# Performance work log

Measured on AMD Instinct MI355X. Metric: run time of the kernel, lower is better.

## Reference

```python
import jax, jax.numpy as jnp
import numpy as np

E, H, I = 8, 2048, 768  # num_experts, hidden_size, moe_intermediate_size
B, S = 4, 1024


def setup_inputs() -> dict:
    key = jax.random.key(0)
    k1, k2, k3, k4, k5 = jax.random.split(key, 5)
    hidden_states = jax.random.normal(k1, (B, S, H), dtype=jnp.float32)
    routing_weights = jax.random.uniform(k2, (B * S, E), dtype=jnp.float32)
    router_indices = jax.random.randint(k3, (B * S, 2), 0, E)
    gate_up_proj = jax.random.normal(k4, (E, H, 2 * I), dtype=jnp.float32) * 0.02
    down_proj = jax.random.normal(k5, (E, I, H), dtype=jnp.float32) * 0.02
    return {
        "hidden_states": hidden_states,
        "routing_weights": routing_weights,
        "router_indices": router_indices,
        "gate_up_proj": gate_up_proj,
        "down_proj": down_proj,
    }


def reference(hidden_states, routing_weights, router_indices, gate_up_proj, down_proj):
    b, s, h = hidden_states.shape
    x = hidden_states.reshape(-1, h)  # [T, H], T = B*S
    # dense all-experts: every token through every expert
    gate_up = jnp.einsum("th,ehd->etd", x, gate_up_proj)  # [E, T, 2I]
    gate, up = jnp.split(gate_up, 2, axis=-1)
    inter = up * jax.nn.silu(gate)  # [E, T, I]
    out = jnp.einsum("eti,eih->eth", inter, down_proj)  # [E, T, H]
    rw = routing_weights.T.reshape(out.shape[0], b, s)  # [E, B, S]
    out = out.reshape(out.shape[0], b, s, h) * rw[..., None]
    return out.sum(axis=0)  # [B, S, H]
```

## Files before the change

### kernel.cpp

```cpp
#include <hip/hip_runtime.h>
#include <cstdint>
#include <cstddef>

#define NE 8
#define NH 2048
#define NI 768
#define NT 4096
#define NK2 6144

typedef __bf16 bf16x8 __attribute__((ext_vector_type(8)));
typedef float f32x4 __attribute__((ext_vector_type(4)));
typedef unsigned short u16x8 __attribute__((ext_vector_type(8)));

__device__ __forceinline__ unsigned short f2bf(float f) {
  unsigned int u = __builtin_bit_cast(unsigned int, f);
  u += 0x7fffu + ((u >> 16) & 1u);
  return (unsigned short)(u >> 16);
}

__device__ __forceinline__ void gload_lds16(const void* g, void* s) {
  __builtin_amdgcn_global_load_lds(
      (const __attribute__((address_space(1))) unsigned int*)g,
      (__attribute__((address_space(3))) unsigned int*)s, 16, 0, 0);
}

__global__ __launch_bounds__(256) void k_cvt(const float* __restrict__ in,
                                             unsigned short* __restrict__ out,
                                             long n) {
  long i = ((long)blockIdx.x * blockDim.x + threadIdx.x) * 8;
  if (i >= n) return;
  float4 f0 = *reinterpret_cast<const float4*>(in + i);
  float4 f1 = *reinterpret_cast<const float4*>(in + i + 4);
  u16x8 o;
  o[0] = f2bf(f0.x); o[1] = f2bf(f0.y); o[2] = f2bf(f0.z); o[3] = f2bf(f0.w);
  o[4] = f2bf(f1.x); o[5] = f2bf(f1.y); o[6] = f2bf(f1.z); o[7] = f2bf(f1.w);
  *reinterpret_cast<u16x8*>(out + i) = o;
}

__global__ __launch_bounds__(256) void k_transpose_cvt(
    const float* __restrict__ in, unsigned short* __restrict__ out,
    int R, int C, long inBS, long outBS, int outCS, int mode) {
  __shared__ float tile[32][33];
  const int b = blockIdx.z;
  const int r0 = blockIdx.y * 32, c0 = blockIdx.x * 32;
  const int tx = threadIdx.x, ty = threadIdx.y;
  const float* ib = in + (long)b * inBS;
#pragma unroll
  for (int d = 0; d < 4; d++)
    tile[ty + d * 8][tx] = ib[(long)(r0 + ty + d * 8) * C + c0 + tx];
  __syncthreads();
#pragma unroll
  for (int d = 0; d < 4; d++) {
    int c = c0 + ty + d * 8;
    int r = r0 + tx;
    int orow;
    if (mode == 1) {
      int z = (c >= NI) ? 1 : 0;
      int cc = c - z * NI;
      orow = ((cc >> 4) << 5) + (z << 4) + (cc & 15);
    } else {
      orow = c;
    }
    out[(long)b * outBS + (long)orow * outCS + r] = f2bf(tile[tx][ty + d * 8]);
  }
}


__global__ __launch_bounds__(512, 1) void k_gemm1(
    const unsigned short* __restrict__ Xb,
    const unsigned short* __restrict__ W1t,
    const float* __restrict__ rw,
    unsigned short* __restrict__ inter) {
  __shared__ unsigned short ldsA[2][16384];
  __shared__ unsigned short ldsB[2][16384];

  const int e = blockIdx.z;
  const int t0 = blockIdx.y * 256;
  const int bn = blockIdx.x;
  const int tid = threadIdx.x;
  const int lane = tid & 63, wave = tid >> 6;
  const int wr = wave >> 2, wc = wave & 3;
  const int fr = lane & 15, fq = lane >> 4;
  const int nkt = NH / 64;

  const unsigned short* Bg = W1t + (size_t)e * (2 * NI) * NH;
  const int rih = tid >> 3, ck = tid & 7;
  const unsigned short* sA = Xb + (size_t)(t0 + rih) * NH + ((ck ^ (rih & 7)) << 3);
  const unsigned short* sB = Bg + (size_t)(bn * 256 + rih) * NH + ((ck ^ (rih & 7)) << 3);
  const int dst = tid * 8;

#define STG1(C) do { \
    const int cc_ = (C); const size_t ko_ = (size_t)cc_ * 64; \
    unsigned short* da_ = &ldsA[cc_ & 1][dst]; \
    unsigned short* db_ = &ldsB[cc_ & 1][dst]; \
    _Pragma("unroll") \
    for (int q = 0; q < 4; ++q) { \
      gload_lds16(sA + ko_ + (size_t)q * (64 * NH), da_ + q * 4096); \
      gload_lds16(sB + ko_ + (size_t)q * (64 * NH), db_ + q * 4096); \
    } \
  } while (0)

  f32x4 acc[8][4];
#pragma unroll
  for (int i = 0; i < 8; ++i)
#pragma unroll
    for (int j = 0; j < 4; ++j) acc[i][j] = (f32x4){0.f, 0.f, 0.f, 0.f};

  const int swz = fr & 7;
  int aoff[8], boff[4];
#pragma unroll
  for (int i = 0; i < 8; ++i)
    aoff[i] = ((i >> 2) * 128 + wr * 64 + (i & 3) * 16 + fr) * 64 + ((fq ^ swz) << 3);
#pragma unroll
  for (int j = 0; j < 4; ++j)
    boff[j] = ((j >> 1) * 128 + wc * 32 + (j & 1) * 16 + fr) * 64 + ((fq ^ swz) << 3);
  const int dk = ((((4 + fq) ^ swz) - (fq ^ swz)) << 3);

  STG1(0);
  asm volatile("s_waitcnt vmcnt(0)" ::: "memory");
  asm volatile("s_barrier" ::: "memory");

  for (int kt = 0; kt < nkt; ++kt) {
    const int cur = kt & 1;
    const unsigned short* lA = ldsA[cur];
    const unsigned short* lB = ldsB[cur];

    bf16x8 af[8][2], bf[4][2];
#pragma unroll
    for (int m = 0; m < 8; ++m) {
      af[m][0] = *reinterpret_cast<const bf16x8*>(lA + aoff[m]);
      af[m][1] = *reinterpret_cast<const bf16x8*>(lA + aoff[m] + dk);
    }
#pragma unroll
    for (int j = 0; j < 4; ++j) {
      bf[j][0] = *reinterpret_cast<const bf16x8*>(lB + boff[j]);
      bf[j][1] = *reinterpret_cast<const bf16x8*>(lB + boff[j] + dk);
    }

    if (kt + 1 < nkt) STG1(kt + 1);

#pragma unroll
    for (int kk = 0; kk < 2; ++kk)
#pragma unroll
      for (int m = 0; m < 8; ++m)
#pragma unroll
        for (int j = 0; j < 4; ++j)
          acc[m][j] = __builtin_amdgcn_mfma_f32_16x16x32_bf16(af[m][kk], bf[j][kk], acc[m][j], 0, 0, 0);

    asm volatile("s_waitcnt vmcnt(0)" ::: "memory");
    asm volatile("s_barrier" ::: "memory");
  }
#undef STG1

#pragma unroll
  for (int i = 0; i < 8; ++i) {
    const int trow = t0 + (i >> 2) * 128 + wr * 64 + (i & 3) * 16 + fq * 4;
#pragma unroll
    for (int r = 0; r < 4; ++r) {
      const int t = trow + r;
      const float rwv = rw[(size_t)t * NE + e];
#pragma unroll
      for (int p = 0; p < 2; ++p) {
        float g = acc[i][2 * p][r];
        float u = acc[i][2 * p + 1][r];
        float s = g / (1.f + __expf(-g));
        const int col = bn * 128 + (p * 4 + wc) * 16 + fr;
        inter[(size_t)t * NK2 + e * NI + col] = f2bf(rwv * u * s);
      }
    }
  }
}

__global__ __launch_bounds__(512, 1) void k_gemm2(
    const unsigned short* __restrict__ inter,
    const unsigned short* __restrict__ W2t,
    float* __restrict__ out) {
  __shared__ unsigned short ldsA[2][16384];
  __shared__ unsigned short ldsB[2][8192];

  const int t0 = blockIdx.y * 256;
  const int h0 = blockIdx.x * 128;
  const int tid = threadIdx.x;
  const int lane = tid & 63, wave = tid >> 6;
  const int wr = wave >> 1, wc = wave & 1;
  const int fr = lane & 15, fq = lane >> 4;
  const int nkt = NK2 / 64;

  const int rih = tid >> 3, ck = tid & 7;
  const unsigned short* sA = inter + (size_t)(t0 + rih) * NK2 + ((ck ^ (rih & 7)) << 3);
  const unsigned short* sB = W2t + (size_t)(h0 + rih) * NK2 + ((ck ^ (rih & 7)) << 3);
  const int dst = tid * 8;

#define STG2(C) do { \
    const int cc_ = (C); \
    unsigned short* da_ = &ldsA[cc_ & 1][dst]; \
    unsigned short* db_ = &ldsB[cc_ & 1][dst]; \
    const size_t ko_ = (size_t)cc_ * 64; \
    _Pragma("unroll") \
    for (int q = 0; q < 4; ++q) \
      gload_lds16(sA + ko_ + (size_t)q * (64 * NK2), da_ + q * 4096); \
    _Pragma("unroll") \
    for (int q = 0; q < 2; ++q) \
      gload_lds16(sB + ko_ + (size_t)q * (64 * NK2), db_ + q * 4096); \
  } while (0)

  f32x4 acc[4][4];
#pragma unroll
  for (int i = 0; i < 4; ++i)
#pragma unroll
    for (int j = 0; j < 4; ++j) acc[i][j] = (f32x4){0.f, 0.f, 0.f, 0.f};

  const int swz = fr & 7;
  int aoff[4], boff[4];
#pragma unroll
  for (int i = 0; i < 4; ++i)
    aoff[i] = (wr * 64 + i * 16 + fr) * 64 + ((fq ^ swz) << 3);
#pragma unroll
  for (int j = 0; j < 4; ++j)
    boff[j] = (wc * 64 + j * 16 + fr) * 64 + ((fq ^ swz) << 3);
  const int dk = ((((4 + fq) ^ swz) - (fq ^ swz)) << 3);

  STG2(0);
  asm volatile("s_waitcnt vmcnt(0)" ::: "memory");
  asm volatile("s_barrier" ::: "memory");

  for (int kt = 0; kt < nkt; ++kt) {
    const int cur = kt & 1;
    const unsigned short* lA = ldsA[cur];
    const unsigned short* lB = ldsB[cur];

    bf16x8 af[4][2], bf[4][2];
#pragma unroll
    for (int i = 0; i < 4; ++i) {
      af[i][0] = *reinterpret_cast<const bf16x8*>(lA + aoff[i]);
      af[i][1] = *reinterpret_cast<const bf16x8*>(lA + aoff[i] + dk);
    }
#pragma unroll
    for (int j = 0; j < 4; ++j) {
      bf[j][0] = *reinterpret_cast<const bf16x8*>(lB + boff[j]);
      bf[j][1] = *reinterpret_cast<const bf16x8*>(lB + boff[j] + dk);
    }

    if (kt + 1 < nkt) STG2(kt + 1);

#pragma unroll
    for (int kk = 0; kk < 2; ++kk)
#pragma unroll
      for (int i = 0; i < 4; ++i)
#pragma unroll
        for (int j = 0; j < 4; ++j)
          acc[i][j] = __builtin_amdgcn_mfma_f32_16x16x32_bf16(af[i][kk], bf[j][kk], acc[i][j], 0, 0, 0);

    asm volatile("s_waitcnt vmcnt(0)" ::: "memory");
    asm volatile("s_barrier" ::: "memory");
  }
#undef STG2

  const int rowBase = t0 + wr * 64 + fq * 4;
#pragma unroll
  for (int i = 0; i < 4; ++i)
#pragma unroll
    for (int j = 0; j < 4; ++j)
#pragma unroll
      for (int r = 0; r < 4; ++r)
        out[(size_t)(rowBase + i * 16 + r) * NH + h0 + wc * 64 + j * 16 + fr] =
            acc[i][j][r];
}

extern "C" void kernel_launch(void* const* d_in, const int* in_sizes, int n_in,
                              void* d_out, int out_size, void* d_ws, size_t ws_size,
                              hipStream_t stream) {
  const float* x = (const float*)d_in[0];
  const float* rw = (const float*)d_in[1];
  const float* w1 = (const float*)d_in[3];
  const float* w2 = (const float*)d_in[4];
  float* out = (float*)d_out;

  char* ws = (char*)d_ws;
  unsigned short* Xb = (unsigned short*)ws;
  unsigned short* W1t = (unsigned short*)(ws + 16777216);
  unsigned short* W2t = (unsigned short*)(ws + 16777216 + 50331648);
  unsigned short* inter = (unsigned short*)(ws + 16777216 + 50331648 + 25165824);

  k_cvt<<<dim3((NT * NH) / (256 * 8)), dim3(256), 0, stream>>>(x, Xb, (long)NT * NH);
  k_transpose_cvt<<<dim3((2 * NI) / 32, NH / 32, NE), dim3(32, 8), 0, stream>>>(
      w1, W1t, NH, 2 * NI, (long)NH * 2 * NI, (long)2 * NI * NH, NH, 1);
  k_transpose_cvt<<<dim3(NH / 32, NI / 32, NE), dim3(32, 8), 0, stream>>>(
      w2, W2t, NI, NH, (long)NI * NH, (long)NI, NK2, 0);
  k_gemm1<<<dim3((2 * NI) / 256, NT / 256, NE), dim3(512), 0, stream>>>(Xb, W1t, rw, inter);
  k_gemm2<<<dim3(NH / 128, NT / 256), dim3(512), 0, stream>>>(inter, W2t, out);
}
```

Baseline: 362.1 us.

## Deepen GEMM pipelines to 4-stage K=32 ring with register double-buffered fragments

Both GEMM kernels switch from a 2-stage, K=64 LDS double buffer with a full vmcnt(0) drain every iteration to a 4-slot LDS ring of K=32 tiles, prefetching three stages ahead. Fragment reads for the next step are issued before the MFMAs of the current step, and the wait uses partial vmcnt counts so global loads overlap compute. The LDS layout is changed to pack two rows per 64-element line with a new XOR swizzle. The cost is twice as many barriers per K, more registers for the two fragment sets, and a riskier wait and slot accounting scheme.

```diff
diff --git a/kernel.cpp b/kernel.cpp
--- a/kernel.cpp
+++ b/kernel.cpp
@@ -71,8 +71,7 @@
     const unsigned short* __restrict__ W1t,
     const float* __restrict__ rw,
     unsigned short* __restrict__ inter) {
-  __shared__ unsigned short ldsA[2][16384];
-  __shared__ unsigned short ldsB[2][16384];
+  __shared__ unsigned short lds[4][16384];
 
   const int e = blockIdx.z;
   const int t0 = blockIdx.y * 256;
@@ -81,23 +80,29 @@
   const int lane = tid & 63, wave = tid >> 6;
   const int wr = wave >> 2, wc = wave & 3;
   const int fr = lane & 15, fq = lane >> 4;
-  const int nkt = NH / 64;
+  const int nkt = NH / 32;
 
   const unsigned short* Bg = W1t + (size_t)e * (2 * NI) * NH;
-  const int rih = tid >> 3, ck = tid & 7;
-  const unsigned short* sA = Xb + (size_t)(t0 + rih) * NH + ((ck ^ (rih & 7)) << 3);
-  const unsigned short* sB = Bg + (size_t)(bn * 256 + rih) * NH + ((ck ^ (rih & 7)) << 3);
-  const int dst = tid * 8;
-
-#define STG1(C) do { \
-    const int cc_ = (C); const size_t ko_ = (size_t)cc_ * 64; \
-    unsigned short* da_ = &ldsA[cc_ & 1][dst]; \
-    unsigned short* db_ = &ldsB[cc_ & 1][dst]; \
-    _Pragma("unroll") \
-    for (int q = 0; q < 4; ++q) { \
-      gload_lds16(sA + ko_ + (size_t)q * (64 * NH), da_ + q * 4096); \
-      gload_lds16(sB + ko_ + (size_t)q * (64 * NH), db_ + q * 4096); \
-    } \
+
+  int r0c, k0c, r1c, k1c;
+  {
+    int c = tid, pr = c >> 3, pc = c & 7, pcl = pc ^ (pr & 7);
+    r0c = (pr << 1) | (pcl >> 2); k0c = pcl & 3;
+    c = tid + 512; pr = c >> 3; pc = c & 7; pcl = pc ^ (pr & 7);
+    r1c = (pr << 1) | (pcl >> 2); k1c = pcl & 3;
+  }
+  const unsigned short* sA0 = Xb + (size_t)(t0 + r0c) * NH + k0c * 8;
+  const unsigned short* sA1 = Xb + (size_t)(t0 + r1c) * NH + k1c * 8;
+  const unsigned short* sB0 = Bg + (size_t)(bn * 256 + r0c) * NH + k0c * 8;
+  const unsigned short* sB1 = Bg + (size_t)(bn * 256 + r1c) * NH + k1c * 8;
+  const int dst0 = tid * 8, dst1 = tid * 8 + 4096;
+
+#define STG1(T) do { \
+    unsigned short* L_ = lds[(T) & 3]; const size_t ko_ = (size_t)(T) * 32; \
+    gload_lds16(sA0 + ko_, L_ + dst0); \
+    gload_lds16(sA1 + ko_, L_ + dst1); \
+    gload_lds16(sB0 + ko_, L_ + 8192 + dst0); \
+    gload_lds16(sB1 + ko_, L_ + 8192 + dst1); \
   } while (0)
 
   f32x4 acc[8][4];
@@ -106,50 +111,57 @@
 #pragma unroll
     for (int j = 0; j < 4; ++j) acc[i][j] = (f32x4){0.f, 0.f, 0.f, 0.f};
 
-  const int swz = fr & 7;
   int aoff[8], boff[4];
 #pragma unroll
-  for (int i = 0; i < 8; ++i)
-    aoff[i] = ((i >> 2) * 128 + wr * 64 + (i & 3) * 16 + fr) * 64 + ((fq ^ swz) << 3);
-#pragma unroll
-  for (int j = 0; j < 4; ++j)
-    boff[j] = ((j >> 1) * 128 + wc * 32 + (j & 1) * 16 + fr) * 64 + ((fq ^ swz) << 3);
-  const int dk = ((((4 + fq) ^ swz) - (fq ^ swz)) << 3);
-
-  STG1(0);
+  for (int m = 0; m < 8; ++m) {
+    const int rA = (m >> 2) * 128 + wr * 64 + (m & 3) * 16 + fr;
+    const int pr = rA >> 1;
+    const int pcs = (((rA & 1) << 2) | fq) ^ (pr & 7);
+    aoff[m] = pr * 64 + pcs * 8;
+  }
+#pragma unroll
+  for (int j = 0; j < 4; ++j) {
+    const int rB = (j >> 1) * 128 + wc * 32 + (j & 1) * 16 + fr;
+    const int pr = rB >> 1;
+    const int pcs = (((rB & 1) << 2) | fq) ^ (pr & 7);
+    boff[j] = 8192 + pr * 64 + pcs * 8;
+  }
+
+#define READ1(T, F) do { \
+    const unsigned short* L_ = lds[(T) & 3]; \
+    _Pragma("unroll") \
+    for (int m = 0; m < 8; ++m) F[m] = *reinterpret_cast<const bf16x8*>(L_ + aoff[m]); \
+    _Pragma("unroll") \
+    for (int j = 0; j < 4; ++j) F[8 + j] = *reinterpret_cast<const bf16x8*>(L_ + boff[j]); \
+  } while (0)
+
+#define REGION1(KT, CUR, NXT) do { \
+    const int kt_ = (KT); \
+    if (kt_ + 1 < nkt) READ1(kt_ + 1, NXT); \
+    if (kt_ + 3 < nkt) STG1(kt_ + 3); \
+    _Pragma("unroll") \
+    for (int m = 0; m < 8; ++m) \
+      _Pragma("unroll") \
+      for (int j = 0; j < 4; ++j) \
+        acc[m][j] = __builtin_amdgcn_mfma_f32_16x16x32_bf16(CUR[m], CUR[8 + j], acc[m][j], 0, 0, 0); \
+    if (kt_ + 3 < nkt)      { asm volatile("s_waitcnt vmcnt(4)" ::: "memory"); } \
+    else if (kt_ + 2 < nkt) { asm volatile("s_waitcnt vmcnt(0)" ::: "memory"); } \
+    if (kt_ + 1 < nkt)      { asm volatile("s_barrier" ::: "memory"); } \
+  } while (0)
+
+  STG1(0); STG1(1); STG1(2);
+  asm volatile("s_waitcnt vmcnt(4)" ::: "memory");
+  asm volatile("s_barrier" ::: "memory");
+
+  bf16x8 fE[12], fO[12];
+  READ1(0, fE);
+  for (int i = 0; i < nkt / 2; ++i) {
+    REGION1(2 * i, fE, fO);
+    REGION1(2 * i + 1, fO, fE);
+  }
   asm volatile("s_waitcnt vmcnt(0)" ::: "memory");
-  asm volatile("s_barrier" ::: "memory");
-
-  for (int kt = 0; kt < nkt; ++kt) {
-    const int cur = kt & 1;
-    const unsigned short* lA = ldsA[cur];
-    const unsigned short* lB = ldsB[cur];
-
-    bf16x8 af[8][2], bf[4][2];
-#pragma unroll
-    for (int m = 0; m < 8; ++m) {
-      af[m][0] = *reinterpret_cast<const bf16x8*>(lA + aoff[m]);
-      af[m][1] = *reinterpret_cast<const bf16x8*>(lA + aoff[m] + dk);
-    }
-#pragma unroll
-    for (int j = 0; j < 4; ++j) {
-      bf[j][0] = *reinterpret_cast<const bf16x8*>(lB + boff[j]);
-      bf[j][1] = *reinterpret_cast<const bf16x8*>(lB + boff[j] + dk);
-    }
-
-    if (kt + 1 < nkt) STG1(kt + 1);
-
-#pragma unroll
-    for (int kk = 0; kk < 2; ++kk)
-#pragma unroll
-      for (int m = 0; m < 8; ++m)
-#pragma unroll
-        for (int j = 0; j < 4; ++j)
-          acc[m][j] = __builtin_amdgcn_mfma_f32_16x16x32_bf16(af[m][kk], bf[j][kk], acc[m][j], 0, 0, 0);
-
-    asm volatile("s_waitcnt vmcnt(0)" ::: "memory");
-    asm volatile("s_barrier" ::: "memory");
-  }
+#undef REGION1
+#undef READ1
 #undef STG1
 
 #pragma unroll
@@ -175,8 +187,7 @@
     const unsigned short* __restrict__ inter,
     const unsigned short* __restrict__ W2t,
     float* __restrict__ out) {
-  __shared__ unsigned short ldsA[2][16384];
-  __shared__ unsigned short ldsB[2][8192];
+  __shared__ unsigned short lds[4][12288];
 
   const int t0 = blockIdx.y * 256;
   const int h0 = blockIdx.x * 128;
@@ -184,24 +195,25 @@
   const int lane = tid & 63, wave = tid >> 6;
   const int wr = wave >> 1, wc = wave & 1;
   const int fr = lane & 15, fq = lane >> 4;
-  const int nkt = NK2 / 64;
-
-  const int rih = tid >> 3, ck = tid & 7;
-  const unsigned short* sA = inter + (size_t)(t0 + rih) * NK2 + ((ck ^ (rih & 7)) << 3);
-  const unsigned short* sB = W2t + (size_t)(h0 + rih) * NK2 + ((ck ^ (rih & 7)) << 3);
-  const int dst = tid * 8;
-
-#define STG2(C) do { \
-    const int cc_ = (C); \
-    unsigned short* da_ = &ldsA[cc_ & 1][dst]; \
-    unsigned short* db_ = &ldsB[cc_ & 1][dst]; \
-    const size_t ko_ = (size_t)cc_ * 64; \
-    _Pragma("unroll") \
-    for (int q = 0; q < 4; ++q) \
-      gload_lds16(sA + ko_ + (size_t)q * (64 * NK2), da_ + q * 4096); \
-    _Pragma("unroll") \
-    for (int q = 0; q < 2; ++q) \
-      gload_lds16(sB + ko_ + (size_t)q * (64 * NK2), db_ + q * 4096); \
+  const int nkt = NK2 / 32;
+
+  int r0c, k0c, r1c, k1c;
+  {
+    int c = tid, pr = c >> 3, pc = c & 7, pcl = pc ^ (pr & 7);
+    r0c = (pr << 1) | (pcl >> 2); k0c = pcl & 3;
+    c = tid + 512; pr = c >> 3; pc = c & 7; pcl = pc ^ (pr & 7);
+    r1c = (pr << 1) | (pcl >> 2); k1c = pcl & 3;
+  }
+  const unsigned short* sA0 = inter + (size_t)(t0 + r0c) * NK2 + k0c * 8;
+  const unsigned short* sA1 = inter + (size_t)(t0 + r1c) * NK2 + k1c * 8;
+  const unsigned short* sB0 = W2t + (size_t)(h0 + r0c) * NK2 + k0c * 8;
+  const int dst0 = tid * 8, dst1 = tid * 8 + 4096;
+
+#define STG2(T) do { \
+    unsigned short* L_ = lds[(T) & 3]; const size_t ko_ = (size_t)(T) * 32; \
+    gload_lds16(sA0 + ko_, L_ + dst0); \
+    gload_lds16(sA1 + ko_, L_ + dst1); \
+    gload_lds16(sB0 + ko_, L_ + 8192 + dst0); \
   } while (0)
 
   f32x4 acc[4][4];
@@ -210,50 +222,57 @@
 #pragma unroll
     for (int j = 0; j < 4; ++j) acc[i][j] = (f32x4){0.f, 0.f, 0.f, 0.f};
 
-  const int swz = fr & 7;
   int aoff[4], boff[4];
 #pragma unroll
-  for (int i = 0; i < 4; ++i)
-    aoff[i] = (wr * 64 + i * 16 + fr) * 64 + ((fq ^ swz) << 3);
-#pragma unroll
-  for (int j = 0; j < 4; ++j)
-    boff[j] = (wc * 64 + j * 16 + fr) * 64 + ((fq ^ swz) << 3);
-  const int dk = ((((4 + fq) ^ swz) - (fq ^ swz)) << 3);
-
-  STG2(0);
+  for (int m = 0; m < 4; ++m) {
+    const int rA = wr * 64 + m * 16 + fr;
+    const int pr = rA >> 1;
+    const int pcs = (((rA & 1) << 2) | fq) ^ (pr & 7);
+    aoff[m] = pr * 64 + pcs * 8;
+  }
+#pragma unroll
+  for (int j = 0; j < 4; ++j) {
+    const int rB = wc * 64 + j * 16 + fr;
+    const int pr = rB >> 1;
+    const int pcs = (((rB & 1) << 2) | fq) ^ (pr & 7);
+    boff[j] = 8192 + pr * 64 + pcs * 8;
+  }
+
+#define READ2(T, F) do { \
+    const unsigned short* L_ = lds[(T) & 3]; \
+    _Pragma("unroll") \
+    for (int m = 0; m < 4; ++m) F[m] = *reinterpret_cast<const bf16x8*>(L_ + aoff[m]); \
+    _Pragma("unroll") \
+    for (int j = 0; j < 4; ++j) F[4 + j] = *reinterpret_cast<const bf16x8*>(L_ + boff[j]); \
+  } while (0)
+
+#define REGION2(KT, CUR, NXT) do { \
+    const int kt_ = (KT); \
+    if (kt_ + 1 < nkt) READ2(kt_ + 1, NXT); \
+    if (kt_ + 3 < nkt) STG2(kt_ + 3); \
+    _Pragma("unroll") \
+    for (int m = 0; m < 4; ++m) \
+      _Pragma("unroll") \
+      for (int j = 0; j < 4; ++j) \
+        acc[m][j] = __builtin_amdgcn_mfma_f32_16x16x32_bf16(CUR[m], CUR[4 + j], acc[m][j], 0, 0, 0); \
+    if (kt_ + 3 < nkt)      { asm volatile("s_waitcnt vmcnt(3)" ::: "memory"); } \
+    else if (kt_ + 2 < nkt) { asm volatile("s_waitcnt vmcnt(0)" ::: "memory"); } \
+    if (kt_ + 1 < nkt)      { asm volatile("s_barrier" ::: "memory"); } \
+  } while (0)
+
+  STG2(0); STG2(1); STG2(2);
+  asm volatile("s_waitcnt vmcnt(3)" ::: "memory");
+  asm volatile("s_barrier" ::: "memory");
+
+  bf16x8 fE[8], fO[8];
+  READ2(0, fE);
+  for (int i = 0; i < nkt / 2; ++i) {
+    REGION2(2 * i, fE, fO);
+    REGION2(2 * i + 1, fO, fE);
+  }
   asm volatile("s_waitcnt vmcnt(0)" ::: "memory");
-  asm volatile("s_barrier" ::: "memory");
-
-  for (int kt = 0; kt < nkt; ++kt) {
-    const int cur = kt & 1;
-    const unsigned short* lA = ldsA[cur];
-    const unsigned short* lB = ldsB[cur];
-
-    bf16x8 af[4][2], bf[4][2];
-#pragma unroll
-    for (int i = 0; i < 4; ++i) {
-      af[i][0] = *reinterpret_cast<const bf16x8*>(lA + aoff[i]);
-      af[i][1] = *reinterpret_cast<const bf16x8*>(lA + aoff[i] + dk);
-    }
-#pragma unroll
-    for (int j = 0; j < 4; ++j) {
-      bf[j][0] = *reinterpret_cast<const bf16x8*>(lB + boff[j]);
-      bf[j][1] = *reinterpret_cast<const bf16x8*>(lB + boff[j] + dk);
-    }
-
-    if (kt + 1 < nkt) STG2(kt + 1);
-
-#pragma unroll
-    for (int kk = 0; kk < 2; ++kk)
-#pragma unroll
-      for (int i = 0; i < 4; ++i)
-#pragma unroll
-        for (int j = 0; j < 4; ++j)
-          acc[i][j] = __builtin_amdgcn_mfma_f32_16x16x32_bf16(af[i][kk], bf[j][kk], acc[i][j], 0, 0, 0);
-
-    asm volatile("s_waitcnt vmcnt(0)" ::: "memory");
-    asm volatile("s_barrier" ::: "memory");
-  }
+#undef REGION2
+#undef READ2
 #undef STG2
 
   const int rowBase = t0 + wr * 64 + fq * 4;
```

Measured after the change: 363.0 us. No clear change (+0.2%).
